# Kernel optimization log

Measured on AMD Instinct MI355X. Metric: run time of the kernel, lower is better.

Reference implementation:

```python
import jax, jax.numpy as jnp
import numpy as np

B, L, D, V, K = 4, 2048, 1024, 32, 4096  # batch, seq, embedding_dim, vq_dim, num_embeddings


def setup_inputs() -> dict:
    key = jax.random.key(0)
    k0, k1, k2, k3 = jax.random.split(key, 4)
    h = jax.random.normal(k0, (B, L, D), jnp.float32)
    attn_mask = jnp.ones((B, L), jnp.float32)
    # proj: Linear(D -> V); proj_inv: Linear(V -> D)
    Wp = jax.random.normal(k1, (V, D), jnp.float32) / np.float32(np.sqrt(D))
    bp = jnp.zeros((V,), jnp.float32)
    Wpi = jax.random.normal(k2, (D, V), jnp.float32) / np.float32(np.sqrt(V))
    bpi = jnp.zeros((D,), jnp.float32)
    # embedding init uniform(-1/K, 1/K)
    emb = jax.random.uniform(k3, (K, V), jnp.float32, -1.0 / K, 1.0 / K)
    return {"h": h, "attn_mask": attn_mask, "Wp": Wp, "bp": bp,
            "Wpi": Wpi, "bpi": bpi, "emb": emb}


def reference(h, attn_mask, Wp, bp, Wpi, bpi, emb, temperature=1.0):
    # project + L2 normalize
    hp = jnp.einsum('bld,vd->blv', h, Wp) + bp            # [B,L,V]
    hp = hp / jnp.linalg.norm(hp, axis=-1, keepdims=True)
    # normalize codebook (in torch this is an in-place .data update)
    emb_n = emb / jnp.linalg.norm(emb, axis=-1, keepdims=True)  # [K,V]
    # squared euclidean distances hp vs codebook
    d = (jnp.sum(hp * hp, axis=-1, keepdims=True)
         + jnp.sum(emb_n * emb_n, axis=-1)
         - 2.0 * jnp.einsum('blv,kv->blk', hp, emb_n))    # [B,L,K]
    A = jax.nn.softmax(-d / temperature, axis=-1)         # [B,L,K]
    code = jnp.argmax(A, axis=-1)                         # [B,L]
    h_vq = jnp.einsum('blk,kv->blv', A, emb_n)            # train mode: A @ embedding
    # masked scatter into zeros is equivalent to masking out unselected positions
    m = (attn_mask == 1)
    quantized = jnp.where(m[..., None], h_vq, jnp.float32(0.0))
    vq_code = jnp.where(m, code, 0).astype(jnp.int32)
    quantized = jnp.einsum('blv,dv->bld', quantized, Wpi) + bpi
    vq_loss = jnp.float32(0.0)
    return quantized, vq_code, vq_loss
```

## Files before the change

kernel.cpp:

```cpp
#include <hip/hip_runtime.h>
#include <hip/hip_bf16.h>
#include <math.h>

#define NTOK 8192
#define DIM  1024
#define VDIM 32
#define KCODES 4096

#define SC 2.8853900817779268f

typedef __attribute__((ext_vector_type(8))) short short8;
typedef __attribute__((ext_vector_type(4))) float f32x4;

#define MFMA16(A,B,C) __builtin_amdgcn_mfma_f32_16x16x32_bf16(A, B, C, 0, 0, 0)

__device__ __forceinline__ unsigned short f2bf(float x) {
    unsigned u = __builtin_bit_cast(unsigned, x);
    u += 0x7FFF + ((u >> 16) & 1);
    return (unsigned short)(u >> 16);
}
__device__ __forceinline__ float bf2f(unsigned short b) {
    unsigned u = ((unsigned)b) << 16;
    return __builtin_bit_cast(float, u);
}
__device__ __forceinline__ float fexp2(float x) {
#if __has_builtin(__builtin_amdgcn_exp2f)
    return __builtin_amdgcn_exp2f(x);
#else
    return __expf(0.6931471805599453f * x);
#endif
}

struct U4 { unsigned x, y, z, w; };

__device__ __forceinline__ void split8(const float* p, short8* H, short8* L) {
    unsigned hh[4], ll[4];
    #pragma unroll
    for (int i = 0; i < 4; ++i) {
        unsigned short a = f2bf(p[2 * i]);
        unsigned short b = f2bf(p[2 * i + 1]);
        hh[i] = (unsigned)a | ((unsigned)b << 16);
        unsigned short la = f2bf(p[2 * i] - bf2f(a));
        unsigned short lb = f2bf(p[2 * i + 1] - bf2f(b));
        ll[i] = (unsigned)la | ((unsigned)lb << 16);
    }
    U4 uh = {hh[0], hh[1], hh[2], hh[3]};
    U4 ul = {ll[0], ll[1], ll[2], ll[3]};
    *H = __builtin_bit_cast(short8, uh);
    *L = __builtin_bit_cast(short8, ul);
}

__device__ __forceinline__ short8 pack8(const float* p) {
    unsigned u[8];
    #pragma unroll
    for (int j = 0; j < 8; ++j) u[j] = __builtin_bit_cast(unsigned, p[j]) + 0x8000u;
    U4 uh;
    uh.x = __builtin_amdgcn_perm(u[1], u[0], 0x07060302);
    uh.y = __builtin_amdgcn_perm(u[3], u[2], 0x07060302);
    uh.z = __builtin_amdgcn_perm(u[5], u[4], 0x07060302);
    uh.w = __builtin_amdgcn_perm(u[7], u[6], 0x07060302);
    return __builtin_bit_cast(short8, uh);
}

__device__ __forceinline__ int lsw(int row, int j) {
    int s = ((row >> 1) ^ (row >> 3)) & 3;
    return row * 40 + ((j ^ s) * 8);
}

#define OFS_E_HI   0
#define OFS_E_LO   131072
#define OFS_ET_HI  262144
#define OFS_WP_HI  393216
#define OFS_WP_LO  425984
#define OFS_WPI_HI 458752
#define OFS_WPI_LO 491520
#define OFS_HP_HI  524288
#define OFS_HP_LO  786432
#define F32_BASE   1048576
#define NSPLIT 8
#define FOFS_HVP 0
#define FOFS_LP  2097152
#define FOFS_AMP 2162688
#define FOFS_AIP 2228224

__global__ __launch_bounds__(256) void k_prep(const float* __restrict__ emb,
                                              const float* __restrict__ Wp,
                                              const float* __restrict__ Wpi,
                                              unsigned short* __restrict__ W,
                                              float* __restrict__ loss_out) {
    __shared__ __align__(16) unsigned short Th[32][72];
    int bid = blockIdx.x, tid = threadIdx.x;
    if (bid < 64) {
        int cb = bid * 64;
        int c = tid >> 2, s = tid & 3;
        const float* src = emb + (size_t)(cb + c) * VDIM + s * 8;
        float4 a = *(const float4*)src;
        float4 b = *(const float4*)(src + 4);
        float ps = a.x*a.x + a.y*a.y + a.z*a.z + a.w*a.w
                 + b.x*b.x + b.y*b.y + b.z*b.z + b.w*b.w;
        ps += __shfl_xor(ps, 1);
        ps += __shfl_xor(ps, 2);
        float inv = 1.0f / sqrtf(ps);
        float vals[8] = {a.x*inv, a.y*inv, a.z*inv, a.w*inv,
                         b.x*inv, b.y*inv, b.z*inv, b.w*inv};
        short8 H, L;
        split8(vals, &H, &L);
        *(short8*)(W + OFS_E_HI + (size_t)(cb + c) * VDIM + s * 8) = H;
        *(short8*)(W + OFS_E_LO + (size_t)(cb + c) * VDIM + s * 8) = L;
        #pragma unroll
        for (int j = 0; j < 8; ++j) Th[s * 8 + j][c] = f2bf(vals[j]);
        __syncthreads();
        int row = tid >> 3, seg = tid & 7;
        *(short8*)(W + OFS_ET_HI + (size_t)row * KCODES + cb + seg * 8) =
            *(const short8*)&Th[row][seg * 8];
        if (bid == 0 && tid == 0) loss_out[0] = 0.0f;
    } else if (bid < 80) {
        int i0 = (bid - 64) * 2048 + tid * 8;
        float4 a = *(const float4*)(Wp + i0);
        float4 b = *(const float4*)(Wp + i0 + 4);
        float vals[8] = {a.x, a.y, a.z, a.w, b.x, b.y, b.z, b.w};
        short8 H, L;
        split8(vals, &H, &L);
        *(short8*)(W + OFS_WP_HI + i0) = H;
        *(short8*)(W + OFS_WP_LO + i0) = L;
    } else {
        int i0 = (bid - 80) * 2048 + tid * 8;
        float4 a = *(const float4*)(Wpi + i0);
        float4 b = *(const float4*)(Wpi + i0 + 4);
        float vals[8] = {a.x, a.y, a.z, a.w, b.x, b.y, b.z, b.w};
        short8 H, L;
        split8(vals, &H, &L);
        *(short8*)(W + OFS_WPI_HI + i0) = H;
        *(short8*)(W + OFS_WPI_LO + i0) = L;
    }
}

__global__ __launch_bounds__(256) void k_proj(const float* __restrict__ h,
                                              const unsigned short* __restrict__ W,
                                              const float* __restrict__ bp,
                                              unsigned short* __restrict__ hp_hi,
                                              unsigned short* __restrict__ hp_lo) {
    __shared__ __align__(16) float red[4][16][36];
    const unsigned short* Wp_hi = W + OFS_WP_HI;
    const unsigned short* Wp_lo = W + OFS_WP_LO;
    int tid = threadIdx.x;
    int w = tid >> 6, l = tid & 63, q = l >> 4, m = l & 15;
    int tok0 = blockIdx.x * 16;
    const f32x4 zero4 = {0.f, 0.f, 0.f, 0.f};
    f32x4 acc0 = zero4, acc1 = zero4;
    const float* hb = h + (size_t)(tok0 + m) * DIM + w * 256 + q * 8;
    const unsigned short* w0h = Wp_hi + (size_t)m * DIM + w * 256 + q * 8;
    const unsigned short* w0l = Wp_lo + (size_t)m * DIM + w * 256 + q * 8;
    const unsigned short* w1h = w0h + (size_t)16 * DIM;
    const unsigned short* w1l = w0l + (size_t)16 * DIM;
    #pragma unroll
    for (int c = 0; c < 8; ++c) {
        float4 a = *(const float4*)(hb + c * 32);
        float4 b = *(const float4*)(hb + c * 32 + 4);
        float va[8] = {a.x, a.y, a.z, a.w, b.x, b.y, b.z, b.w};
        short8 Bh, Bl;
        split8(va, &Bh, &Bl);
        short8 A0h = *(const short8*)(w0h + c * 32);
        short8 A0l = *(const short8*)(w0l + c * 32);
        short8 A1h = *(const short8*)(w1h + c * 32);
        short8 A1l = *(const short8*)(w1l + c * 32);
        acc0 = MFMA16(A0l, Bl, acc0); acc0 = MFMA16(A0l, Bh, acc0);
        acc0 = MFMA16(A0h, Bl, acc0); acc0 = MFMA16(A0h, Bh, acc0);
        acc1 = MFMA16(A1l, Bl, acc1); acc1 = MFMA16(A1l, Bh, acc1);
        acc1 = MFMA16(A1h, Bl, acc1); acc1 = MFMA16(A1h, Bh, acc1);
    }
    *(f32x4*)&red[w][m][4 * q]      = acc0;
    *(f32x4*)&red[w][m][16 + 4 * q] = acc1;
    __syncthreads();
    #pragma unroll
    for (int half = 0; half < 2; ++half) {
        int t = (tid >> 5) + half * 8, v = tid & 31;
        float s = bp[v];
        #pragma unroll
        for (int j = 0; j < 4; ++j) s += red[j][t][v];
        float sq = s * s;
        #pragma unroll
        for (int off = 1; off < 32; off <<= 1) sq += __shfl_xor(sq, off);
        float nv = s * (SC / sqrtf(sq));
        unsigned short hb2 = f2bf(nv);
        size_t idx = (size_t)(tok0 + t) * VDIM + v;
        hp_hi[idx] = hb2;
        hp_lo[idx] = f2bf(nv - bf2f(hb2));
    }
}

__global__ __launch_bounds__(256, 2) void k_vq(const unsigned short* __restrict__ W,
                                               float* __restrict__ hvp,
                                               float* __restrict__ lp,
                                               float* __restrict__ amp,
                                               int* __restrict__ aip) {
    __shared__ __align__(16) unsigned short Eh[2][64 * 40];
    __shared__ __align__(16) unsigned short El[2][64 * 40];

    const unsigned short* E_hi  = W + OFS_E_HI;
    const unsigned short* E_lo  = W + OFS_E_LO;
    const unsigned short* Et_hi = W + OFS_ET_HI;
    const unsigned short* hp_hi = W + OFS_HP_HI;
    const unsigned short* hp_lo = W + OFS_HP_LO;

    int tid = threadIdx.x;
    int w = tid >> 6, l = tid & 63, q = l >> 4, m = l & 15;
    int tg = blockIdx.x >> 3, sp = blockIdx.x & 7;
    int tok0 = tg * 128 + w * 32;
    int cb0 = sp * 512;
    int sig = ((m & 12) << 1) | (m & 3);
    const f32x4 zero4 = {0.f, 0.f, 0.f, 0.f};

    int cs = tid >> 2, js = tid & 3;
    int lds_off = lsw(cs, js);
    size_t gs = (size_t)cs * VDIM + js * 8;

    size_t h0 = (size_t)(tok0 + m) * VDIM + q * 8;
    short8 hph0 = *(const short8*)(hp_hi + h0);
    short8 hpl0 = *(const short8*)(hp_lo + h0);
    short8 hph1 = *(const short8*)(hp_hi + h0 + 16 * VDIM);
    short8 hpl1 = *(const short8*)(hp_lo + h0 + 16 * VDIM);

    {
        size_t tb = (size_t)cb0 * VDIM;
        short8 a = *(const short8*)(E_hi + tb + gs);
        short8 b = *(const short8*)(E_lo + tb + gs);
        *(short8*)&Eh[0][lds_off] = a;
        *(short8*)&El[0][lds_off] = b;
    }
    __syncthreads();

    f32x4 hv00 = zero4, hv01 = zero4, hv10 = zero4, hv11 = zero4;
    float ls0 = 0.f, ls1 = 0.f, am0 = -1e30f, am1 = -1e30f;
    int ai0 = 0, ai1 = 0;

    size_t tA = (size_t)sig * KCODES + cb0 + q * 8;
    short8 T0h = *(const short8*)(Et_hi + tA);
    short8 T1h = *(const short8*)(Et_hi + tA + (size_t)4 * KCODES);

    #pragma unroll 1
    for (int t = 0; t < 8; ++t) {
        int buf = t & 1;
        short8 sa, sb;
        if (t < 7) {
            size_t tb = (size_t)(cb0 + (t + 1) * 64) * VDIM;
            sa = *(const short8*)(E_hi + tb + gs);
            sb = *(const short8*)(E_lo + tb + gs);
        }
        #pragma unroll
        for (int cc = 0; cc < 2; ++cc) {
            int cbase = cb0 + t * 64 + cc * 32;
            size_t tN = (size_t)sig * KCODES + (cbase + 32) + q * 8;
            short8 nT0h = *(const short8*)(Et_hi + tN);
            short8 nT1h = *(const short8*)(Et_hi + tN + (size_t)4 * KCODES);
            int r0 = cc * 32 + sig;
            short8 E0h = *(const short8*)&Eh[buf][lsw(r0, q)];
            short8 E0l = *(const short8*)&El[buf][lsw(r0, q)];
            short8 E1h = *(const short8*)&Eh[buf][lsw(r0 + 4, q)];
            short8 E1l = *(const short8*)&El[buf][lsw(r0 + 4, q)];
            int lbase = cbase + 8 * q;

            {
                f32x4 s0 = MFMA16(E0h, hpl0, zero4);
                s0 = MFMA16(E0l, hph0, s0);
                s0 = MFMA16(E0h, hph0, s0);
                f32x4 s1 = MFMA16(E1h, hpl0, zero4);
                s1 = MFMA16(E1l, hph0, s1);
                s1 = MFMA16(E1h, hph0, s1);
                float p[8];
                #pragma unroll
                for (int r = 0; r < 4; ++r) {
                    p[r]     = fexp2(s0[r]);
                    p[4 + r] = fexp2(s1[r]);
                }
                short8 Ph = pack8(p);
                hv00 = MFMA16(T0h, Ph, hv00);
                hv01 = MFMA16(T1h, Ph, hv01);
                #pragma unroll
                for (int r = 0; r < 4; ++r) {
                    float sv = s0[r];
                    if (sv > am0) { am0 = sv; ai0 = lbase + r; }
                    sv = s1[r];
                    if (sv > am0) { am0 = sv; ai0 = lbase + 4 + r; }
                }
                ls0 += ((p[0] + p[1]) + (p[2] + p[3])) + ((p[4] + p[5]) + (p[6] + p[7]));
            }
            {
                f32x4 s0 = MFMA16(E0h, hpl1, zero4);
                s0 = MFMA16(E0l, hph1, s0);
                s0 = MFMA16(E0h, hph1, s0);
                f32x4 s1 = MFMA16(E1h, hpl1, zero4);
                s1 = MFMA16(E1l, hph1, s1);
                s1 = MFMA16(E1h, hph1, s1);
                float p[8];
                #pragma unroll
                for (int r = 0; r < 4; ++r) {
                    p[r]     = fexp2(s0[r]);
                    p[4 + r] = fexp2(s1[r]);
                }
                short8 Ph = pack8(p);
                hv10 = MFMA16(T0h, Ph, hv10);
                hv11 = MFMA16(T1h, Ph, hv11);
                #pragma unroll
                for (int r = 0; r < 4; ++r) {
                    float sv = s0[r];
                    if (sv > am1) { am1 = sv; ai1 = lbase + r; }
                    sv = s1[r];
                    if (sv > am1) { am1 = sv; ai1 = lbase + 4 + r; }
                }
                ls1 += ((p[0] + p[1]) + (p[2] + p[3])) + ((p[4] + p[5]) + (p[6] + p[7]));
            }
            T0h = nT0h; T1h = nT1h;
        }
        if (t < 7) {
            int nb = buf ^ 1;
            *(short8*)&Eh[nb][lds_off] = sa;
            *(short8*)&El[nb][lds_off] = sb;
            __syncthreads();
        }
    }

    #pragma unroll
    for (int off = 16; off <= 32; off <<= 1) {
        ls0 += __shfl_xor(ls0, off);
        float a2 = __shfl_xor(am0, off);
        int   i2 = __shfl_xor(ai0, off);
        if (a2 > am0 || (a2 == am0 && i2 < ai0)) { am0 = a2; ai0 = i2; }
        ls1 += __shfl_xor(ls1, off);
        a2 = __shfl_xor(am1, off);
        i2 = __shfl_xor(ai1, off);
        if (a2 > am1 || (a2 == am1 && i2 < ai1)) { am1 = a2; ai1 = i2; }
    }
    size_t gtok = (size_t)sp * NTOK + tok0;
    if (q == 0) {
        lp[gtok + m] = ls0;      amp[gtok + m] = am0;      aip[gtok + m] = ai0;
        lp[gtok + 16 + m] = ls1; amp[gtok + 16 + m] = am1; aip[gtok + 16 + m] = ai1;
    }
    float* dst0 = hvp + (gtok + m) * VDIM;
    *(f32x4*)(dst0 + 8 * q)     = hv00;
    *(f32x4*)(dst0 + 8 * q + 4) = hv01;
    float* dst1 = hvp + (gtok + 16 + m) * VDIM;
    *(f32x4*)(dst1 + 8 * q)     = hv10;
    *(f32x4*)(dst1 + 8 * q + 4) = hv11;
}

__global__ __launch_bounds__(256) void k_out(const unsigned short* __restrict__ W,
                                             const float* __restrict__ mask,
                                             const float* __restrict__ bpi,
                                             const float* __restrict__ hvp,
                                             const float* __restrict__ lp,
                                             const float* __restrict__ amp,
                                             const int* __restrict__ aip,
                                             float* __restrict__ out,
                                             float* __restrict__ code_out) {
    __shared__ float invl[16];
    __shared__ float lred[16][9];
    __shared__ float amred[16][9];
    __shared__ int   aired[16][9];
    __shared__ __align__(16) unsigned short hvh[16][40];
    __shared__ __align__(16) unsigned short hvl[16][40];
    const unsigned short* Wpi_hi = W + OFS_WPI_HI;
    const unsigned short* Wpi_lo = W + OFS_WPI_LO;
    int tid = threadIdx.x;
    int tok0 = blockIdx.x * 16;
    const f32x4 zero4 = {0.f, 0.f, 0.f, 0.f};

    if (tid < 128) {
        int t = tid >> 3, s = tid & 7;
        size_t gi = (size_t)s * NTOK + tok0 + t;
        lred[t][s]  = lp[gi];
        amred[t][s] = amp[gi];
        aired[t][s] = aip[gi];
    }
    __syncthreads();
    if (tid < 16) {
        float L = 0.f, A = -1e30f;
        int I = 0x7fffffff;
        #pragma unroll
        for (int s = 0; s < NSPLIT; ++s) {
            L += lred[tid][s];
            float a2 = amred[tid][s];
            int   i2 = aired[tid][s];
            if (a2 > A || (a2 == A && i2 < I)) { A = a2; I = i2; }
        }
        bool on = (mask[tok0 + tid] == 1.0f);
        code_out[tok0 + tid] = on ? (float)I : 0.0f;
        invl[tid] = on ? (1.0f / L) : 0.0f;
    }
    __syncthreads();
    #pragma unroll
    for (int it = 0; it < 2; ++it) {
        int idx = it * 256 + tid;
        int t = idx >> 5, v = idx & 31;
        float x = 0.f;
        #pragma unroll
        for (int sp = 0; sp < NSPLIT; ++sp)
            x += hvp[((size_t)sp * NTOK + tok0 + t) * VDIM + v];
        x *= invl[t];
        unsigned short hb = f2bf(x);
        hvh[t][v] = hb;
        hvl[t][v] = f2bf(x - bf2f(hb));
    }
    __syncthreads();
    int w = tid >> 6, l = tid & 63, q = l >> 4, m = l & 15;
    short8 gh = *(const short8*)&hvh[m][q * 8];
    short8 gl = *(const short8*)&hvl[m][q * 8];
    #pragma unroll
    for (int dt = 0; dt < 16; ++dt) {
        int dbase = w * 256 + dt * 16;
        short8 Ah = *(const short8*)(Wpi_hi + (size_t)(dbase + m) * VDIM + q * 8);
        short8 Al = *(const short8*)(Wpi_lo + (size_t)(dbase + m) * VDIM + q * 8);
        f32x4 o = MFMA16(Al, gh, zero4);
        o = MFMA16(Ah, gl, o);
        o = MFMA16(Ah, gh, o);
        float4 bias = *(const float4*)(bpi + dbase + 4 * q);
        float4 r0 = make_float4(o[0] + bias.x, o[1] + bias.y,
                                o[2] + bias.z, o[3] + bias.w);
        *(float4*)(out + (size_t)(tok0 + m) * DIM + dbase + 4 * q) = r0;
    }
}

extern "C" void kernel_launch(void* const* d_in, const int* in_sizes, int n_in,
                              void* d_out, int out_size, void* d_ws, size_t ws_size,
                              hipStream_t stream) {
    const float* h    = (const float*)d_in[0];
    const float* mask = (const float*)d_in[1];
    const float* Wp   = (const float*)d_in[2];
    const float* bp   = (const float*)d_in[3];
    const float* Wpi  = (const float*)d_in[4];
    const float* bpi  = (const float*)d_in[5];
    const float* emb  = (const float*)d_in[6];
    float* out = (float*)d_out;

    unsigned short* W = (unsigned short*)d_ws;
    unsigned short* hp_hi = W + OFS_HP_HI;
    unsigned short* hp_lo = W + OFS_HP_LO;
    float* fbase = (float*)(W + F32_BASE);
    float* hvp = fbase + FOFS_HVP;
    float* lpp = fbase + FOFS_LP;
    float* ampp = fbase + FOFS_AMP;
    int*   aipp = (int*)(fbase + FOFS_AIP);

    float* code_out = out + (size_t)NTOK * DIM;
    float* loss_out = code_out + NTOK;

    hipLaunchKernelGGL(k_prep, dim3(96),  dim3(256), 0, stream, emb, Wp, Wpi, W, loss_out);
    hipLaunchKernelGGL(k_proj, dim3(512), dim3(256), 0, stream, h, W, bp, hp_hi, hp_lo);
    hipLaunchKernelGGL(k_vq,   dim3(512), dim3(256), 0, stream, W, hvp, lpp, ampp, aipp);
    hipLaunchKernelGGL(k_out,  dim3(512), dim3(256), 0, stream, W, mask, bpi, hvp, lpp, ampp, aipp, out, code_out);
}
```

Baseline: 134.1 us.

## Reduce codebook-split partials with global atomics instead of per-split buffers

Each of the 8 codebook-split blocks in the VQ kernel now atomically adds its softmax-weighted sums and denominators into a single per-token buffer. It also merges argmax through a 64-bit packed key with atomicMax, replacing the 8-way partial arrays that the output kernel used to reduce. The prep kernel gains blocks that zero these accumulators. The aim is to cut partial-buffer traffic and the reduction loop in k_out, at the cost of many float atomics and nondeterministic summation order. The denominator accumulation is also packed into float2 vectors.

```diff
diff --git a/kernel.cpp b/kernel.cpp
--- a/kernel.cpp
+++ b/kernel.cpp
@@ -11,6 +11,7 @@
 
 typedef __attribute__((ext_vector_type(8))) short short8;
 typedef __attribute__((ext_vector_type(4))) float f32x4;
+typedef __attribute__((ext_vector_type(2))) float f32x2;
 
 #define MFMA16(A,B,C) __builtin_amdgcn_mfma_f32_16x16x32_bf16(A, B, C, 0, 0, 0)
 
@@ -29,6 +30,16 @@
 #else
     return __expf(0.6931471805599453f * x);
 #endif
+}
+
+__device__ __forceinline__ unsigned fmono(float x) {
+    unsigned u = __builtin_bit_cast(unsigned, x);
+    unsigned s = (u & 0x80000000u) ? 0xFFFFFFFFu : 0x80000000u;
+    return u ^ s;
+}
+__device__ __forceinline__ unsigned long long amkey(float am, int ai) {
+    return ((unsigned long long)fmono(am) << 32) |
+           (unsigned long long)(0xFFFFFFFFu - (unsigned)ai);
 }
 
 struct U4 { unsigned x, y, z, w; };
@@ -75,13 +86,11 @@
 #define OFS_WPI_HI 458752
 #define OFS_WPI_LO 491520
 #define OFS_HP_HI  524288
-#define OFS_HP_LO  786432
 #define F32_BASE   1048576
-#define NSPLIT 8
-#define FOFS_HVP 0
-#define FOFS_LP  2097152
-#define FOFS_AMP 2162688
-#define FOFS_AIP 2228224
+#define FOFS_HV  0
+#define FOFS_L   262144
+#define FOFS_KEY 270336
+#define ZERO_F4  71680
 
 __global__ __launch_bounds__(256) void k_prep(const float* __restrict__ emb,
                                               const float* __restrict__ Wp,
@@ -123,7 +132,7 @@
         split8(vals, &H, &L);
         *(short8*)(W + OFS_WP_HI + i0) = H;
         *(short8*)(W + OFS_WP_LO + i0) = L;
-    } else {
+    } else if (bid < 96) {
         int i0 = (bid - 80) * 2048 + tid * 8;
         float4 a = *(const float4*)(Wpi + i0);
         float4 b = *(const float4*)(Wpi + i0 + 4);
@@ -132,6 +141,11 @@
         split8(vals, &H, &L);
         *(short8*)(W + OFS_WPI_HI + i0) = H;
         *(short8*)(W + OFS_WPI_LO + i0) = L;
+    } else {
+        int t = (bid - 96) * 256 + tid;
+        float4* f4 = (float4*)(W + F32_BASE);
+        const float4 z = make_float4(0.f, 0.f, 0.f, 0.f);
+        for (int i = t; i < ZERO_F4; i += 8192) f4[i] = z;
     }
 }
 
@@ -190,10 +204,9 @@
 }
 
 __global__ __launch_bounds__(256, 2) void k_vq(const unsigned short* __restrict__ W,
-                                               float* __restrict__ hvp,
-                                               float* __restrict__ lp,
-                                               float* __restrict__ amp,
-                                               int* __restrict__ aip) {
+                                               float* __restrict__ hv,
+                                               float* __restrict__ Lm,
+                                               unsigned long long* __restrict__ Km) {
     __shared__ __align__(16) unsigned short Eh[2][64 * 40];
     __shared__ __align__(16) unsigned short El[2][64 * 40];
 
@@ -201,7 +214,7 @@
     const unsigned short* E_lo  = W + OFS_E_LO;
     const unsigned short* Et_hi = W + OFS_ET_HI;
     const unsigned short* hp_hi = W + OFS_HP_HI;
-    const unsigned short* hp_lo = W + OFS_HP_LO;
+    const unsigned short* hp_lo = W + OFS_HP_HI + NTOK * VDIM;
 
     int tid = threadIdx.x;
     int w = tid >> 6, l = tid & 63, q = l >> 4, m = l & 15;
@@ -231,7 +244,8 @@
     __syncthreads();
 
     f32x4 hv00 = zero4, hv01 = zero4, hv10 = zero4, hv11 = zero4;
-    float ls0 = 0.f, ls1 = 0.f, am0 = -1e30f, am1 = -1e30f;
+    f32x2 ls0v = {0.f, 0.f}, ls1v = {0.f, 0.f};
+    float am0 = -1e30f, am1 = -1e30f;
     int ai0 = 0, ai1 = 0;
 
     size_t tA = (size_t)sig * KCODES + cb0 + q * 8;
@@ -283,7 +297,9 @@
                     sv = s1[r];
                     if (sv > am0) { am0 = sv; ai0 = lbase + 4 + r; }
                 }
-                ls0 += ((p[0] + p[1]) + (p[2] + p[3])) + ((p[4] + p[5]) + (p[6] + p[7]));
+                f32x2 pa = {p[0], p[1]}, pb = {p[2], p[3]};
+                f32x2 pc = {p[4], p[5]}, pd = {p[6], p[7]};
+                ls0v += (pa + pb) + (pc + pd);
             }
             {
                 f32x4 s0 = MFMA16(E0h, hpl1, zero4);
@@ -308,7 +324,9 @@
                     sv = s1[r];
                     if (sv > am1) { am1 = sv; ai1 = lbase + 4 + r; }
                 }
-                ls1 += ((p[0] + p[1]) + (p[2] + p[3])) + ((p[4] + p[5]) + (p[6] + p[7]));
+                f32x2 pa = {p[0], p[1]}, pb = {p[2], p[3]};
+                f32x2 pc = {p[4], p[5]}, pd = {p[6], p[7]};
+                ls1v += (pa + pb) + (pc + pd);
             }
             T0h = nT0h; T1h = nT1h;
         }
@@ -320,6 +338,8 @@
         }
     }
 
+    float ls0 = ls0v.x + ls0v.y;
+    float ls1 = ls1v.x + ls1v.y;
     #pragma unroll
     for (int off = 16; off <= 32; off <<= 1) {
         ls0 += __shfl_xor(ls0, off);
@@ -331,32 +351,32 @@
         i2 = __shfl_xor(ai1, off);
         if (a2 > am1 || (a2 == am1 && i2 < ai1)) { am1 = a2; ai1 = i2; }
     }
-    size_t gtok = (size_t)sp * NTOK + tok0;
     if (q == 0) {
-        lp[gtok + m] = ls0;      amp[gtok + m] = am0;      aip[gtok + m] = ai0;
-        lp[gtok + 16 + m] = ls1; amp[gtok + 16 + m] = am1; aip[gtok + 16 + m] = ai1;
-    }
-    float* dst0 = hvp + (gtok + m) * VDIM;
-    *(f32x4*)(dst0 + 8 * q)     = hv00;
-    *(f32x4*)(dst0 + 8 * q + 4) = hv01;
-    float* dst1 = hvp + (gtok + 16 + m) * VDIM;
-    *(f32x4*)(dst1 + 8 * q)     = hv10;
-    *(f32x4*)(dst1 + 8 * q + 4) = hv11;
+        unsafeAtomicAdd(&Lm[tok0 + m], ls0);
+        atomicMax(&Km[tok0 + m], amkey(am0, ai0));
+        unsafeAtomicAdd(&Lm[tok0 + 16 + m], ls1);
+        atomicMax(&Km[tok0 + 16 + m], amkey(am1, ai1));
+    }
+    float* dst0 = hv + (size_t)(tok0 + m) * VDIM + 8 * q;
+    float* dst1 = hv + (size_t)(tok0 + 16 + m) * VDIM + 8 * q;
+    #pragma unroll
+    for (int r = 0; r < 4; ++r) {
+        unsafeAtomicAdd(dst0 + r,     hv00[r]);
+        unsafeAtomicAdd(dst0 + 4 + r, hv01[r]);
+        unsafeAtomicAdd(dst1 + r,     hv10[r]);
+        unsafeAtomicAdd(dst1 + 4 + r, hv11[r]);
+    }
 }
 
 __global__ __launch_bounds__(256) void k_out(const unsigned short* __restrict__ W,
                                              const float* __restrict__ mask,
                                              const float* __restrict__ bpi,
-                                             const float* __restrict__ hvp,
-                                             const float* __restrict__ lp,
-                                             const float* __restrict__ amp,
-                                             const int* __restrict__ aip,
+                                             const float* __restrict__ hv,
+                                             const float* __restrict__ Lm,
+                                             const unsigned long long* __restrict__ Km,
                                              float* __restrict__ out,
                                              float* __restrict__ code_out) {
     __shared__ float invl[16];
-    __shared__ float lred[16][9];
-    __shared__ float amred[16][9];
-    __shared__ int   aired[16][9];
     __shared__ __align__(16) unsigned short hvh[16][40];
     __shared__ __align__(16) unsigned short hvl[16][40];
     const unsigned short* Wpi_hi = W + OFS_WPI_HI;
@@ -365,24 +385,10 @@
     int tok0 = blockIdx.x * 16;
     const f32x4 zero4 = {0.f, 0.f, 0.f, 0.f};
 
-    if (tid < 128) {
-        int t = tid >> 3, s = tid & 7;
-        size_t gi = (size_t)s * NTOK + tok0 + t;
-        lred[t][s]  = lp[gi];
-        amred[t][s] = amp[gi];
-        aired[t][s] = aip[gi];
-    }
-    __syncthreads();
     if (tid < 16) {
-        float L = 0.f, A = -1e30f;
-        int I = 0x7fffffff;
-        #pragma unroll
-        for (int s = 0; s < NSPLIT; ++s) {
-            L += lred[tid][s];
-            float a2 = amred[tid][s];
-            int   i2 = aired[tid][s];
-            if (a2 > A || (a2 == A && i2 < I)) { A = a2; I = i2; }
-        }
+        float L = Lm[tok0 + tid];
+        unsigned long long k = Km[tok0 + tid];
+        int I = (int)(0xFFFFFFFFu - (unsigned)(k & 0xFFFFFFFFu));
         bool on = (mask[tok0 + tid] == 1.0f);
         code_out[tok0 + tid] = on ? (float)I : 0.0f;
         invl[tid] = on ? (1.0f / L) : 0.0f;
@@ -392,11 +398,7 @@
     for (int it = 0; it < 2; ++it) {
         int idx = it * 256 + tid;
         int t = idx >> 5, v = idx & 31;
-        float x = 0.f;
-        #pragma unroll
-        for (int sp = 0; sp < NSPLIT; ++sp)
-            x += hvp[((size_t)sp * NTOK + tok0 + t) * VDIM + v];
-        x *= invl[t];
+        float x = hv[(size_t)(tok0 + t) * VDIM + v] * invl[t];
         unsigned short hb = f2bf(x);
         hvh[t][v] = hb;
         hvl[t][v] = f2bf(x - bf2f(hb));
@@ -434,18 +436,17 @@
 
     unsigned short* W = (unsigned short*)d_ws;
     unsigned short* hp_hi = W + OFS_HP_HI;
-    unsigned short* hp_lo = W + OFS_HP_LO;
+    unsigned short* hp_lo = W + OFS_HP_HI + NTOK * VDIM;
     float* fbase = (float*)(W + F32_BASE);
-    float* hvp = fbase + FOFS_HVP;
-    float* lpp = fbase + FOFS_LP;
-    float* ampp = fbase + FOFS_AMP;
-    int*   aipp = (int*)(fbase + FOFS_AIP);
+    float* hv = fbase + FOFS_HV;
+    float* Lm = fbase + FOFS_L;
+    unsigned long long* Km = (unsigned long long*)(fbase + FOFS_KEY);
 
     float* code_out = out + (size_t)NTOK * DIM;
     float* loss_out = code_out + NTOK;
 
-    hipLaunchKernelGGL(k_prep, dim3(96),  dim3(256), 0, stream, emb, Wp, Wpi, W, loss_out);
+    hipLaunchKernelGGL(k_prep, dim3(128), dim3(256), 0, stream, emb, Wp, Wpi, W, loss_out);
     hipLaunchKernelGGL(k_proj, dim3(512), dim3(256), 0, stream, h, W, bp, hp_hi, hp_lo);
-    hipLaunchKernelGGL(k_vq,   dim3(512), dim3(256), 0, stream, W, hvp, lpp, ampp, aipp);
-    hipLaunchKernelGGL(k_out,  dim3(512), dim3(256), 0, stream, W, mask, bpi, hvp, lpp, ampp, aipp, out, code_out);
-}
+    hipLaunchKernelGGL(k_vq,   dim3(512), dim3(256), 0, stream, W, hv, Lm, Km);
+    hipLaunchKernelGGL(k_out,  dim3(512), dim3(256), 0, stream, W, mask, bpi, hv, Lm, Km, out, code_out);
+}
```

New measurement: 182.5 us. 36.2% more time.
